# Optimization experiments

Measured on AMD Instinct MI355X. Metric: run time of the kernel, lower is better.

Reference implementation:

```python
import jax, jax.numpy as jnp
import numpy as np

N_NODES = 100000
N_EDGES = 1600000
D_FEAT = 64
D_HID = 128
N_HOP = 3


def setup_inputs() -> dict:
    key = jax.random.key(0)
    ks = jax.random.split(key, 7)
    nodes = jax.random.normal(ks[0], (N_NODES, D_FEAT), dtype=jnp.float32)
    senders = jax.random.randint(ks[1], (N_EDGES,), 0, N_NODES, dtype=jnp.int32)
    receivers = jax.random.randint(ks[2], (N_EDGES,), 0, N_NODES, dtype=jnp.int32)
    # per-hop MLP params (n_hop=3 independent layers), lecun-style scaling
    W1 = jax.random.normal(ks[3], (N_HOP, D_FEAT, D_HID), dtype=jnp.float32) / np.sqrt(D_FEAT)
    b1 = jnp.zeros((N_HOP, D_HID), dtype=jnp.float32)
    W2 = jax.random.normal(ks[4], (N_HOP, D_HID, D_FEAT), dtype=jnp.float32) / np.sqrt(D_HID)
    b2 = jnp.zeros((N_HOP, D_FEAT), dtype=jnp.float32)
    return {"nodes": nodes, "senders": senders, "receivers": receivers,
            "W1": W1, "b1": b1, "W2": W2, "b2": b2}


def _gcn_hop(x, senders, receivers, w1, b1, w2, b2):
    # update_node_fn: 2-layer MLP with leaky_relu between layers
    x = jax.nn.leaky_relu(jnp.dot(x, w1) + b1)
    x = jnp.dot(x, w2) + b2
    n = x.shape[0]
    ones = jnp.ones(senders.shape, dtype=x.dtype)
    send_deg = jax.ops.segment_sum(ones, senders, num_segments=n)
    recv_deg = jax.ops.segment_sum(ones, receivers, num_segments=n)
    # symmetric normalization: D_s^{-1/2} gather -> scatter-sum -> D_r^{-1/2}
    x = x * jax.lax.rsqrt(jnp.maximum(send_deg, 1.0))[:, None]
    x = jax.ops.segment_sum(x[senders], receivers, num_segments=n)
    x = x * jax.lax.rsqrt(jnp.maximum(recv_deg, 1.0))[:, None]
    return x


def reference(nodes, senders, receivers, W1, b1, W2, b2):
    x = nodes
    for i in range(N_HOP):
        x = _gcn_hop(x, senders, receivers, W1[i], b1[i], W2[i], b2[i])
    return x
```

## Files before the change

### kernel.cpp

```cpp
#include <hip/hip_runtime.h>

#define LRELU_SLOPE 0.01f
#define NBLK_A 512
#define BIN_SZ 256
#define MAXBIN 5120
#define NC2 128

typedef unsigned short ushort_t;
typedef unsigned int uint_t;

typedef float f32x4 __attribute__((ext_vector_type(4)));
typedef short bf16x8 __attribute__((ext_vector_type(8)));
#define MFMA16(a, b, c) __builtin_amdgcn_mfma_f32_16x16x32_bf16(a, b, c, 0, 0, 0)

__device__ inline uint_t f2bf(float f) {
    unsigned u = __float_as_uint(f);
    return (u + 0x7FFFu + ((u >> 16) & 1u)) >> 16;
}

__device__ inline void split2(float v, uint_t& hi, uint_t& lo) {
    hi = f2bf(v);
    float hif = __uint_as_float(hi << 16);
    lo = f2bf(v - hif);
}

__device__ inline float4 bf4_to_f4(ushort4 v) {
    float4 r;
    r.x = __uint_as_float((unsigned)v.x << 16);
    r.y = __uint_as_float((unsigned)v.y << 16);
    r.z = __uint_as_float((unsigned)v.z << 16);
    r.w = __uint_as_float((unsigned)v.w << 16);
    return r;
}

__device__ inline void acc_bf8(uint4 v, float* a) {
    a[0] += __uint_as_float(v.x << 16);
    a[1] += __uint_as_float(v.x & 0xFFFF0000u);
    a[2] += __uint_as_float(v.y << 16);
    a[3] += __uint_as_float(v.y & 0xFFFF0000u);
    a[4] += __uint_as_float(v.z << 16);
    a[5] += __uint_as_float(v.z & 0xFFFF0000u);
    a[6] += __uint_as_float(v.w << 16);
    a[7] += __uint_as_float(v.w & 0xFFFF0000u);
}

__device__ inline void acc_bf8m(uint4 v, float ok, float* a) {
    a[0] = fmaf(__uint_as_float(v.x << 16), ok, a[0]);
    a[1] = fmaf(__uint_as_float(v.x & 0xFFFF0000u), ok, a[1]);
    a[2] = fmaf(__uint_as_float(v.y << 16), ok, a[2]);
    a[3] = fmaf(__uint_as_float(v.y & 0xFFFF0000u), ok, a[3]);
    a[4] = fmaf(__uint_as_float(v.z << 16), ok, a[4]);
    a[5] = fmaf(__uint_as_float(v.z & 0xFFFF0000u), ok, a[5]);
    a[6] = fmaf(__uint_as_float(v.w << 16), ok, a[6]);
    a[7] = fmaf(__uint_as_float(v.w & 0xFFFF0000u), ok, a[7]);
}


__global__ __launch_bounds__(256) void build1_kernel(
        const float* __restrict__ W1, const float* __restrict__ W2,
        ushort_t* __restrict__ w1p, ushort_t* __restrict__ w2p,
        const int* __restrict__ receivers, int* __restrict__ cntA, int csA,
        const int* __restrict__ senders, uint_t* __restrict__ hist, int cs2,
        int e, int nbins, int half, int nwords) {
    __shared__ uint_t lds[12544];
    int bid = blockIdx.x, t = threadIdx.x;
    if (bid < 3) {
        int hop = bid;
        const float* w1 = W1 + hop * 64 * 128;
        const float* w2 = W2 + hop * 128 * 64;
        ushort_t* p1h = w1p + (size_t)hop * 16384;
        ushort_t* p1l = p1h + 8192;
        ushort_t* p2h = w2p + (size_t)hop * 16384;
        ushort_t* p2l = p2h + 8192;
        for (int i = t; i < 8192; i += 256) {
            int j = i & 7, o = (i >> 3) & 127, cq = i >> 10;
            int k = (cq >> 2) * 32 + (cq & 3) * 8 + j;
            uint_t h, l;
            split2(w1[k * 128 + o], h, l);
            p1h[i] = (ushort_t)h; p1l[i] = (ushort_t)l;
        }
        for (int i = t; i < 8192; i += 256) {
            int j = i & 7, o = (i >> 3) & 63, cq = i >> 9;
            int k = (cq >> 2) * 32 + (cq & 3) * 8 + j;
            uint_t h, l;
            split2(w2[k * 64 + o], h, l);
            p2h[i] = (ushort_t)h; p2l[i] = (ushort_t)l;
        }
    } else if (bid < 3 + NBLK_A) {
        int* cnt = (int*)lds;
        int b = bid - 3;
        for (int i = t; i < nbins; i += 256) cnt[i] = 0;
        __syncthreads();
        int base = b * csA, lim = min(csA, e - base);
        for (int i = t; i < lim; i += 256)
            atomicAdd(&cnt[receivers[base + i] >> 8], 1);
        __syncthreads();
        for (int i = t; i < nbins; i += 256) cntA[b * nbins + i] = cnt[i];
    } else {
        int idx = bid - 3 - NBLK_A;
        int c = idx >> 1;
        int h = idx & 1;
        int hw = half >> 2;
        for (int i = t; i < hw; i += 256) lds[i] = 0;
        __syncthreads();
        int base = c * cs2, lim = min(cs2, e - base);
        int lo = h * half;
        for (int i = t; i < lim; i += 256) {
            int v = senders[base + i] - lo;
            if ((unsigned)v < (unsigned)half)
                atomicAdd(&lds[v >> 2], 1u << ((v & 3) * 8));
        }
        __syncthreads();
        uint_t* d = hist + (size_t)c * nwords + (size_t)h * hw;
        for (int i = t; i < hw; i += 256) d[i] = lds[i];
    }
}


__global__ __launch_bounds__(512) void build2_kernel(
        const int* __restrict__ cntA, int* __restrict__ offT,
        int* __restrict__ binTot, int nbins,
        const uint_t* __restrict__ hist, int* __restrict__ deg,
        int nwords, int n) {
    __shared__ int s[NBLK_A];
    int bid = blockIdx.x, t = threadIdx.x;
    if (bid < nbins) {
        int bin = bid;
        int v = cntA[t * nbins + bin];
        s[t] = v;
        __syncthreads();
        for (int off = 1; off < NBLK_A; off <<= 1) {
            int add = (t >= off) ? s[t - off] : 0;
            __syncthreads();
            s[t] += add;
            __syncthreads();
        }
        offT[bin * NBLK_A + t] = s[t] - v;
        if (t == NBLK_A - 1) binTot[bin] = s[t];
    } else {
        int w = (bid - nbins) * 512 + t;
        if (w >= nwords) return;
        uint_t run = 0;
        for (int c = 0; c < NC2; c++) run += hist[(size_t)c * nwords + w];
        int v = w * 4;
        if (v + 3 < n) {
            ((int4*)deg)[w] = make_int4(run & 255, (run >> 8) & 255,
                                        (run >> 16) & 255, (int)(run >> 24));
        } else {
            for (int j = 0; j < 4 && v + j < n; j++) deg[v + j] = (run >> (8 * j)) & 255;
        }
    }
}

__global__ __launch_bounds__(512) void scanb_kernel(const int* __restrict__ binTot,
        int* __restrict__ binStart, int nbins) {
    __shared__ int s[512];
    int t = threadIdx.x;
    int v = (t < nbins) ? binTot[t] : 0;
    s[t] = v;
    __syncthreads();
    for (int off = 1; off < 512; off <<= 1) {
        int add = (t >= off) ? s[t - off] : 0;
        __syncthreads();
        s[t] += add;
        __syncthreads();
    }
    if (t < nbins) binStart[t] = s[t] - v;
    if (t == nbins - 1) binStart[nbins] = s[t];
}

__global__ __launch_bounds__(256) void binscat_kernel(const int* __restrict__ keys,
        const int* __restrict__ payload, const int* __restrict__ offT,
        const int* __restrict__ binStart,
        uint2* __restrict__ pairs, int cs, int e, int nbins) {
    __shared__ int cur[512];
    int b = blockIdx.x, t = threadIdx.x;
    for (int i = t; i < nbins; i += 256) cur[i] = offT[i * NBLK_A + b] + binStart[i];
    __syncthreads();
    int base = b * cs, lim = min(cs, e - base);
    for (int i = t; i < lim; i += 256) {
        int k = keys[base + i];
        int pl = payload[base + i];
        int pos = atomicAdd(&cur[k >> 8], 1);
        pairs[pos] = make_uint2((unsigned)k, (unsigned)pl);
    }
}

__global__ __launch_bounds__(256) void binsort_kernel(const uint2* __restrict__ pairs,
        const int* __restrict__ binStart, int* __restrict__ row_start,
        int* __restrict__ bucket, int nbins, int n, int e) {
    __shared__ int cnt[BIN_SZ];
    __shared__ int loc[BIN_SZ];
    __shared__ int buf[MAXBIN];
    int bin = blockIdx.x, t = threadIdx.x;
    int e0 = binStart[bin], e1 = binStart[bin + 1];
    int m = e1 - e0;
    if (m > MAXBIN) m = MAXBIN;
    cnt[t] = 0;
    __syncthreads();
    for (int i = t; i < m; i += 256)
        atomicAdd(&cnt[pairs[e0 + i].x & 255], 1);
    __syncthreads();
    int v = cnt[t];
    int node = bin * BIN_SZ + t;
    loc[t] = v;
    __syncthreads();
    for (int off = 1; off < BIN_SZ; off <<= 1) {
        int add = (t >= off) ? loc[t - off] : 0;
        __syncthreads();
        loc[t] += add;
        __syncthreads();
    }
    int excl = loc[t] - v;
    if (node < n) row_start[node] = e0 + excl;
    if (bin == nbins - 1 && t == 255) row_start[n] = e;
    cnt[t] = excl;
    __syncthreads();
    for (int i = t; i < m; i += 256) {
        uint2 pr = pairs[e0 + i];
        int pos = atomicAdd(&cnt[pr.x & 255], 1);
        buf[pos] = (int)pr.y;
    }
    __syncthreads();
    for (int i = t; i < m; i += 256) bucket[e0 + i] = buf[i];
}


template<int GATHER>
__global__ __launch_bounds__(512) void fused_mlp_kernel(const float* __restrict__ x,
        const ushort_t* __restrict__ yin, const int* __restrict__ rs,
        const int* __restrict__ bucket,
        const ushort_t* __restrict__ w1p, const float* __restrict__ b1g,
        const ushort_t* __restrict__ w2p, const float* __restrict__ b2g,
        const int* __restrict__ sdeg, ushort_t* __restrict__ y, int n) {
    __shared__ __align__(16) char smem[54272];
    ushort_t* xsh = (ushort_t*)smem;
    ushort_t* xsl = xsh + 4608;
    ushort_t* hsh = xsl + 4608;
    ushort_t* hsl = hsh + 8704;
    float* b1f   = (float*)(hsl + 8704);
    float* b2f   = b1f + 128;
    float* snorm = b2f + 64;
    float* ybuf  = (float*)smem;

    const ushort_t* w1ph = w1p;
    const ushort_t* w1pl = w1p + 8192;
    const ushort_t* w2ph = w2p;
    const ushort_t* w2pl = w2p + 8192;

    int tid = threadIdx.x;
    int nb = blockIdx.x * 64;

    if (tid < 32) ((float4*)b1f)[tid] = ((const float4*)b1g)[tid];
    else if (tid < 48) ((float4*)b2f)[tid - 32] = ((const float4*)b2g)[tid - 32];
    if (tid >= 448) {
        int t = tid - 448;
        int gn = nb + t;
        int d = (gn < n) ? sdeg[gn] : 1;
        snorm[t] = rsqrtf(fmaxf((float)d, 1.0f));
    }

    if (GATHER) {
        int node = tid >> 3, j = tid & 7;
        int gn = nb + node;
        float a[8];
        #pragma unroll
        for (int k = 0; k < 8; k++) a[k] = 0.f;
        if (gn < n) {
            int s0 = rs[gn];
            int deg = rs[gn + 1] - s0;
            const uint4* yrow = (const uint4*)yin;
            int i = 0;
            for (; i + 16 <= deg; i += 16) {
                int idx[16];
                #pragma unroll
                for (int k = 0; k < 16; k++) idx[k] = bucket[s0 + i + k];
                uint4 r0[16];
                #pragma unroll
                for (int k = 0; k < 16; k++) r0[k] = yrow[(size_t)idx[k] * 8 + j];
                #pragma unroll
                for (int k = 0; k < 16; k++) acc_bf8(r0[k], a);
            }
            for (; i < deg; i += 8) {
                int idx[8]; float ok[8];
                #pragma unroll
                for (int k = 0; k < 8; k++) {
                    int ii = i + k;
                    bool v = ii < deg;
                    idx[k] = bucket[v ? s0 + ii : s0];
                    ok[k] = v ? 1.0f : 0.0f;
                }
                uint4 rr[8];
                #pragma unroll
                for (int k = 0; k < 8; k++) rr[k] = yrow[(size_t)idx[k] * 8 + j];
                #pragma unroll
                for (int k = 0; k < 8; k++) acc_bf8m(rr[k], ok[k], a);
            }
            float sc = rsqrtf(fmaxf((float)deg, 1.0f));
            #pragma unroll
            for (int k = 0; k < 8; k++) a[k] *= sc;
        }
        uint_t h[8], l[8];
        #pragma unroll
        for (int k = 0; k < 8; k++) split2(a[k], h[k], l[k]);
        uint4 oh, ol;
        oh.x = h[0] | (h[1] << 16); oh.y = h[2] | (h[3] << 16);
        oh.z = h[4] | (h[5] << 16); oh.w = h[6] | (h[7] << 16);
        ol.x = l[0] | (l[1] << 16); ol.y = l[2] | (l[3] << 16);
        ol.z = l[4] | (l[5] << 16); ol.w = l[6] | (l[7] << 16);
        *(uint4*)&xsh[node * 72 + j * 8] = oh;
        *(uint4*)&xsl[node * 72 + j * 8] = ol;
    } else {
        for (int i = tid; i < 1024; i += 512) {
            int node = i >> 4, c4 = i & 15;
            int gn = nb + node;
            float4 v = make_float4(0.f, 0.f, 0.f, 0.f);
            if (gn < n) v = ((const float4*)x)[(size_t)gn * 16 + c4];
            uint_t h0, l0, h1, l1, h2, l2, h3, l3;
            split2(v.x, h0, l0); split2(v.y, h1, l1);
            split2(v.z, h2, l2); split2(v.w, h3, l3);
            *(uint2*)&xsh[node * 72 + c4 * 4] = make_uint2(h0 | (h1 << 16), h2 | (h3 << 16));
            *(uint2*)&xsl[node * 72 + c4 * 4] = make_uint2(l0 | (l1 << 16), l2 | (l3 << 16));
        }
    }
    __syncthreads();

    int w = tid >> 6, lane = tid & 63;
    int q = lane >> 4, m = lane & 15;
    int oq = w & 3, nh = w >> 2;
    bool even = ((m & 1) == 0);

    {
        f32x4 acc[2][2];
        #pragma unroll
        for (int a = 0; a < 2; a++)
            #pragma unroll
            for (int b = 0; b < 2; b++) acc[a][b] = (f32x4)(0.f);

        #pragma unroll
        for (int c = 0; c < 2; c++) {
            bf16x8 Ah[2], Al[2];
            #pragma unroll
            for (int nt = 0; nt < 2; nt++) {
                int node = nh * 32 + nt * 16 + m;
                Ah[nt] = *(const bf16x8*)&xsh[node * 72 + c * 32 + q * 8];
                Al[nt] = *(const bf16x8*)&xsl[node * 72 + c * 32 + q * 8];
            }
            #pragma unroll
            for (int ot = 0; ot < 2; ot++) {
                int o1 = oq * 32 + ot * 16 + m;
                size_t fo = (size_t)((c * 4 + q) * 128 + o1) * 8;
                bf16x8 Bh = *(const bf16x8*)&w1ph[fo];
                bf16x8 Bl = *(const bf16x8*)&w1pl[fo];
                #pragma unroll
                for (int nt = 0; nt < 2; nt++) {
                    acc[ot][nt] = MFMA16(Ah[nt], Bh, acc[ot][nt]);
                    acc[ot][nt] = MFMA16(Ah[nt], Bl, acc[ot][nt]);
                    acc[ot][nt] = MFMA16(Al[nt], Bh, acc[ot][nt]);
                }
            }
        }
        float b1v[2];
        b1v[0] = b1f[oq * 32 + m];
        b1v[1] = b1f[oq * 32 + 16 + m];
        #pragma unroll
        for (int ot = 0; ot < 2; ot++)
            #pragma unroll
            for (int nt = 0; nt < 2; nt++) {
                float hv[4], pv[4];
                #pragma unroll
                for (int r = 0; r < 4; r++) {
                    float t = acc[ot][nt][r] + b1v[ot];
                    hv[r] = (t > 0.f) ? t : LRELU_SLOPE * t;
                }
                #pragma unroll
                for (int r = 0; r < 4; r++) pv[r] = __shfl_xor(hv[r], 1, 64);
                int kpos = oq * 32 + ot * 16 + (m & ~1);
                #pragma unroll
                for (int rr = 0; rr < 2; rr++) {
                    int r = even ? rr : (2 + rr);
                    float vlo = even ? hv[r] : pv[r];
                    float vhi = even ? pv[r] : hv[r];
                    uint_t ah, al, bh, bl;
                    split2(vlo, ah, al);
                    split2(vhi, bh, bl);
                    int node = nh * 32 + nt * 16 + 4 * q + r;
                    *(uint_t*)&hsh[node * 136 + kpos] = ah | (bh << 16);
                    *(uint_t*)&hsl[node * 136 + kpos] = al | (bl << 16);
                }
            }
    }
    __syncthreads();

    {
        int ot2 = oq;
        f32x4 acc2[2];
        acc2[0] = (f32x4)(0.f);
        acc2[1] = (f32x4)(0.f);
        #pragma unroll
        for (int c = 0; c < 4; c++) {
            int o2 = ot2 * 16 + m;
            size_t fo = (size_t)((c * 4 + q) * 64 + o2) * 8;
            bf16x8 Bh = *(const bf16x8*)&w2ph[fo];
            bf16x8 Bl = *(const bf16x8*)&w2pl[fo];
            #pragma unroll
            for (int nt = 0; nt < 2; nt++) {
                int node = nh * 32 + nt * 16 + m;
                bf16x8 Ah = *(const bf16x8*)&hsh[node * 136 + c * 32 + q * 8];
                bf16x8 Al = *(const bf16x8*)&hsl[node * 136 + c * 32 + q * 8];
                acc2[nt] = MFMA16(Ah, Bh, acc2[nt]);
                acc2[nt] = MFMA16(Ah, Bl, acc2[nt]);
                acc2[nt] = MFMA16(Al, Bh, acc2[nt]);
            }
        }
        float b2v = b2f[ot2 * 16 + m];
        #pragma unroll
        for (int nt = 0; nt < 2; nt++)
            #pragma unroll
            for (int r = 0; r < 4; r++) {
                int node = nh * 32 + nt * 16 + 4 * q + r;
                float sn = snorm[node];
                ybuf[node * 68 + ot2 * 16 + m] = (acc2[nt][r] + b2v) * sn;
            }
    }
    __syncthreads();

    {
        int node = tid >> 3, c8 = tid & 7;
        int gn = nb + node;
        if (gn < n) {
            const float* src = &ybuf[node * 68 + c8 * 8];
            float4 v0 = *(const float4*)src;
            float4 v1 = *(const float4*)(src + 4);
            uint4 o;
            o.x = f2bf(v0.x) | (f2bf(v0.y) << 16);
            o.y = f2bf(v0.z) | (f2bf(v0.w) << 16);
            o.z = f2bf(v1.x) | (f2bf(v1.y) << 16);
            o.w = f2bf(v1.z) | (f2bf(v1.w) << 16);
            ((uint4*)y)[(size_t)gn * 8 + c8] = o;
        }
    }
}


__global__ __launch_bounds__(256) void agg_kernel(const ushort_t* __restrict__ y,
        const int* __restrict__ rs, const int* __restrict__ bucket,
        float* __restrict__ dst, int n) {
    int wid  = (blockIdx.x * 256 + threadIdx.x) >> 6;
    int lane = threadIdx.x & 63;
    int nd   = lane >> 5;
    int slot = (lane >> 4) & 1;
    int f4   = lane & 15;
    int node = wid * 2 + nd;
    if (node >= n) return;
    int s0  = rs[node];
    int deg = rs[node + 1] - s0;
    const ushort4* y4 = (const ushort4*)y;
    float4 acc = make_float4(0.f, 0.f, 0.f, 0.f);
    for (int i = slot; i < deg; i += 16) {
        int idx[8]; float ok[8];
        #pragma unroll
        for (int j = 0; j < 8; j++) {
            int ii = i + 2 * j;
            bool v = ii < deg;
            idx[j] = bucket[v ? s0 + ii : s0];
            ok[j] = v ? 1.0f : 0.0f;
        }
        #pragma unroll
        for (int j = 0; j < 8; j++) {
            float4 v4 = bf4_to_f4(y4[(size_t)idx[j] * 16 + f4]);
            acc.x = fmaf(v4.x, ok[j], acc.x);
            acc.y = fmaf(v4.y, ok[j], acc.y);
            acc.z = fmaf(v4.z, ok[j], acc.z);
            acc.w = fmaf(v4.w, ok[j], acc.w);
        }
    }
    acc.x += __shfl_xor(acc.x, 16, 64);
    acc.y += __shfl_xor(acc.y, 16, 64);
    acc.z += __shfl_xor(acc.z, 16, 64);
    acc.w += __shfl_xor(acc.w, 16, 64);
    if (slot == 0) {
        float sc = rsqrtf(fmaxf((float)deg, 1.0f));
        acc.x *= sc; acc.y *= sc; acc.z *= sc; acc.w *= sc;
        ((float4*)dst)[(size_t)node * 16 + f4] = acc;
    }
}


extern "C" void kernel_launch(void* const* d_in, const int* in_sizes, int n_in,
                              void* d_out, int out_size, void* d_ws, size_t ws_size,
                              hipStream_t stream) {
    const float* nodes     = (const float*)d_in[0];
    const int*   senders   = (const int*)d_in[1];
    const int*   receivers = (const int*)d_in[2];
    const float* W1 = (const float*)d_in[3];
    const float* b1 = (const float*)d_in[4];
    const float* W2 = (const float*)d_in[5];
    const float* b2 = (const float*)d_in[6];

    int N = in_sizes[0] / 64;
    int E = in_sizes[1];
    int NBINS = (N + BIN_SZ - 1) / BIN_SZ;
    int CSA = (E + NBLK_A - 1) / NBLK_A;
    int CS2 = (E + NC2 - 1) / NC2;
    int HALF = ((N + 7) / 8) * 4;
    int NW2 = 2 * (HALF >> 2);

    char* p = (char*)d_ws;
    auto carve = [&](size_t bytes) -> char* {
        char* r = p;
        p += (bytes + 255) & ~(size_t)255;
        return r;
    };
    ushort_t* yA   = (ushort_t*)carve((size_t)N * 64 * 2);
    ushort_t* yB   = (ushort_t*)carve((size_t)N * 64 * 2);
    int*      rs   = (int*)carve((size_t)(N + 1) * 4);
    int*      sdeg = (int*)carve((size_t)N * 4);
    int*      bucket = (int*)carve((size_t)E * 4);
    int*      binStart = (int*)carve((size_t)(NBINS + 1) * 4);
    int*      binTot   = (int*)carve((size_t)NBINS * 4);
    ushort_t* w1p  = (ushort_t*)carve((size_t)3 * 16384 * 2);
    ushort_t* w2p  = (ushort_t*)carve((size_t)3 * 16384 * 2);
    char* scratch  = carve((size_t)E * 8 + 2 * (size_t)NBLK_A * NBINS * 4 + 4096);
    uint2* pairs = (uint2*)scratch;
    int*   cntA  = (int*)(scratch + (size_t)E * 8);
    int*   offT  = cntA + (size_t)NBLK_A * NBINS;
    uint_t* T1   = (uint_t*)pairs;

    build1_kernel<<<3 + NBLK_A + NC2 * 2, 256, 0, stream>>>(
            W1, W2, w1p, w2p, receivers, cntA, CSA,
            senders, T1, CS2, E, NBINS, HALF, NW2);
    build2_kernel<<<NBINS + (NW2 + 511) / 512, 512, 0, stream>>>(
            cntA, offT, binTot, NBINS, T1, sdeg, NW2, N);
    scanb_kernel<<<1, 512, 0, stream>>>(binTot, binStart, NBINS);
    binscat_kernel<<<NBLK_A, 256, 0, stream>>>(receivers, senders, offT, binStart, pairs, CSA, E, NBINS);
    binsort_kernel<<<NBINS, 256, 0, stream>>>(pairs, binStart, rs, bucket, NBINS, N, E);

    int mbf = (N + 63) / 64;
    int agg_blocks = (N / 2 + 4) / 4 + 1;

    fused_mlp_kernel<0><<<mbf, 512, 0, stream>>>(nodes, nullptr, nullptr, nullptr,
            w1p, b1, w2p, b2, sdeg, yA, N);
    fused_mlp_kernel<1><<<mbf, 512, 0, stream>>>(nullptr, yA, rs, bucket,
            w1p + 16384, b1 + 128, w2p + 16384, b2 + 64, sdeg, yB, N);
    fused_mlp_kernel<1><<<mbf, 512, 0, stream>>>(nullptr, yB, rs, bucket,
            w1p + 32768, b1 + 256, w2p + 32768, b2 + 128, sdeg, yA, N);
    agg_kernel<<<agg_blocks, 256, 0, stream>>>(yA, rs, bucket, (float*)d_out, N);
}
```

Baseline: 330.9 us.

## Build CSR via per-node degree histograms and global atomic scatter

Replaces the two-level bin-partition sort (bin counts, per-bin offsets, pair scatter, per-bin local sort) with receiver degree histograms computed the same way as sender degrees. A scan then gives row starts, and edges are scattered into buckets through global atomicAdd on per-node cursors. This removes the intermediate pairs buffer and the binsort pass, but it adds heavy global atomic contention and produces a nondeterministic order of edges within each row. That ordering could change floating-point summation order in later aggregation.

```diff
diff --git a/kernel.cpp b/kernel.cpp
--- a/kernel.cpp
+++ b/kernel.cpp
@@ -1,9 +1,6 @@
 #include <hip/hip_runtime.h>
 
 #define LRELU_SLOPE 0.01f
-#define NBLK_A 512
-#define BIN_SZ 256
-#define MAXBIN 5120
 #define NC2 128
 
 typedef unsigned short ushort_t;
@@ -59,9 +56,9 @@
 __global__ __launch_bounds__(256) void build1_kernel(
         const float* __restrict__ W1, const float* __restrict__ W2,
         ushort_t* __restrict__ w1p, ushort_t* __restrict__ w2p,
-        const int* __restrict__ receivers, int* __restrict__ cntA, int csA,
-        const int* __restrict__ senders, uint_t* __restrict__ hist, int cs2,
-        int e, int nbins, int half, int nwords) {
+        const int* __restrict__ receivers, uint_t* __restrict__ histR,
+        const int* __restrict__ senders, uint_t* __restrict__ histS,
+        int cs2, int e, int half, int nwords) {
     __shared__ uint_t lds[12544];
     int bid = blockIdx.x, t = threadIdx.x;
     if (bid < 3) {
@@ -86,78 +83,83 @@
             split2(w2[k * 64 + o], h, l);
             p2h[i] = (ushort_t)h; p2l[i] = (ushort_t)l;
         }
-    } else if (bid < 3 + NBLK_A) {
-        int* cnt = (int*)lds;
-        int b = bid - 3;
-        for (int i = t; i < nbins; i += 256) cnt[i] = 0;
-        __syncthreads();
-        int base = b * csA, lim = min(csA, e - base);
-        for (int i = t; i < lim; i += 256)
-            atomicAdd(&cnt[receivers[base + i] >> 8], 1);
-        __syncthreads();
-        for (int i = t; i < nbins; i += 256) cntA[b * nbins + i] = cnt[i];
-    } else {
-        int idx = bid - 3 - NBLK_A;
-        int c = idx >> 1;
-        int h = idx & 1;
-        int hw = half >> 2;
-        for (int i = t; i < hw; i += 256) lds[i] = 0;
-        __syncthreads();
-        int base = c * cs2, lim = min(cs2, e - base);
-        int lo = h * half;
-        for (int i = t; i < lim; i += 256) {
-            int v = senders[base + i] - lo;
-            if ((unsigned)v < (unsigned)half)
-                atomicAdd(&lds[v >> 2], 1u << ((v & 3) * 8));
-        }
-        __syncthreads();
-        uint_t* d = hist + (size_t)c * nwords + (size_t)h * hw;
-        for (int i = t; i < hw; i += 256) d[i] = lds[i];
-    }
+        return;
+    }
+    int role = bid - 3;
+    const int* keys = (role < NC2 * 2) ? receivers : senders;
+    uint_t* hist    = (role < NC2 * 2) ? histR : histS;
+    int idx = (role < NC2 * 2) ? role : role - NC2 * 2;
+    int c = idx >> 1;
+    int h = idx & 1;
+    int hw = half >> 2;
+    for (int i = t; i < hw; i += 256) lds[i] = 0;
+    __syncthreads();
+    int base = c * cs2, lim = min(cs2, e - base);
+    int lo = h * half;
+    for (int i = t; i < lim; i += 256) {
+        int v = keys[base + i] - lo;
+        if ((unsigned)v < (unsigned)half)
+            atomicAdd(&lds[v >> 2], 1u << ((v & 3) * 8));
+    }
+    __syncthreads();
+    uint_t* d = hist + (size_t)c * nwords + (size_t)h * hw;
+    for (int i = t; i < hw; i += 256) d[i] = lds[i];
 }
 
 
 __global__ __launch_bounds__(512) void build2_kernel(
-        const int* __restrict__ cntA, int* __restrict__ offT,
-        int* __restrict__ binTot, int nbins,
-        const uint_t* __restrict__ hist, int* __restrict__ deg,
-        int nwords, int n) {
-    __shared__ int s[NBLK_A];
+        const uint_t* __restrict__ histS, int* __restrict__ sdeg,
+        const uint_t* __restrict__ histR, int* __restrict__ rdeg,
+        int* __restrict__ partials, int ks, int nwords, int n) {
+    __shared__ int s[512];
     int bid = blockIdx.x, t = threadIdx.x;
-    if (bid < nbins) {
-        int bin = bid;
-        int v = cntA[t * nbins + bin];
-        s[t] = v;
-        __syncthreads();
-        for (int off = 1; off < NBLK_A; off <<= 1) {
-            int add = (t >= off) ? s[t - off] : 0;
-            __syncthreads();
-            s[t] += add;
-            __syncthreads();
-        }
-        offT[bin * NBLK_A + t] = s[t] - v;
-        if (t == NBLK_A - 1) binTot[bin] = s[t];
-    } else {
-        int w = (bid - nbins) * 512 + t;
+    if (bid < ks) {
+        int w = bid * 512 + t;
         if (w >= nwords) return;
         uint_t run = 0;
-        for (int c = 0; c < NC2; c++) run += hist[(size_t)c * nwords + w];
+        for (int c = 0; c < NC2; c++) run += histS[(size_t)c * nwords + w];
         int v = w * 4;
         if (v + 3 < n) {
-            ((int4*)deg)[w] = make_int4(run & 255, (run >> 8) & 255,
-                                        (run >> 16) & 255, (int)(run >> 24));
+            ((int4*)sdeg)[w] = make_int4(run & 255, (run >> 8) & 255,
+                                         (run >> 16) & 255, (int)(run >> 24));
         } else {
-            for (int j = 0; j < 4 && v + j < n; j++) deg[v + j] = (run >> (8 * j)) & 255;
-        }
-    }
-}
-
-__global__ __launch_bounds__(512) void scanb_kernel(const int* __restrict__ binTot,
-        int* __restrict__ binStart, int nbins) {
+            for (int j = 0; j < 4 && v + j < n; j++) sdeg[v + j] = (run >> (8 * j)) & 255;
+        }
+    } else {
+        int b2 = bid - ks;
+        int w = b2 * 512 + t;
+        uint_t run = 0;
+        if (w < nwords)
+            for (int c = 0; c < NC2; c++) run += histR[(size_t)c * nwords + w];
+        int d0 = run & 255, d1 = (run >> 8) & 255, d2 = (run >> 16) & 255, d3 = (int)(run >> 24);
+        if (w < nwords) ((int4*)rdeg)[w] = make_int4(d0, d1, d2, d3);
+        s[t] = d0 + d1 + d2 + d3;
+        __syncthreads();
+        for (int off = 256; off > 0; off >>= 1) {
+            if (t < off) s[t] += s[t + off];
+            __syncthreads();
+        }
+        if (t == 0) partials[b2] = s[0];
+    }
+}
+
+
+__global__ __launch_bounds__(512) void scan2_kernel(const int* __restrict__ rdeg,
+        const int* __restrict__ partials, int* __restrict__ rs, int* __restrict__ cursor,
+        int ks, int nwords, int n, int e) {
     __shared__ int s[512];
-    int t = threadIdx.x;
-    int v = (t < nbins) ? binTot[t] : 0;
-    s[t] = v;
+    __shared__ int ps[64];
+    int b = blockIdx.x, t = threadIdx.x;
+    if (t < 64) ps[t] = (t < ks) ? partials[t] : 0;
+    __syncthreads();
+    int base = 0;
+    for (int i = 0; i < b; i++) base += ps[i];
+    __syncthreads();
+    int w = b * 512 + t;
+    int4 d = make_int4(0, 0, 0, 0);
+    if (w < nwords) d = ((const int4*)rdeg)[w];
+    int tot = d.x + d.y + d.z + d.w;
+    s[t] = tot;
     __syncthreads();
     for (int off = 1; off < 512; off <<= 1) {
         int add = (t >= off) ? s[t - off] : 0;
@@ -165,64 +167,33 @@
         s[t] += add;
         __syncthreads();
     }
-    if (t < nbins) binStart[t] = s[t] - v;
-    if (t == nbins - 1) binStart[nbins] = s[t];
-}
-
-__global__ __launch_bounds__(256) void binscat_kernel(const int* __restrict__ keys,
-        const int* __restrict__ payload, const int* __restrict__ offT,
-        const int* __restrict__ binStart,
-        uint2* __restrict__ pairs, int cs, int e, int nbins) {
-    __shared__ int cur[512];
+    int excl = base + s[t] - tot;
+    if (w < nwords) {
+        int v = w * 4;
+        int r0 = excl, r1 = r0 + d.x, r2 = r1 + d.y, r3 = r2 + d.z;
+        if (v + 3 < n) {
+            ((int4*)rs)[w] = make_int4(r0, r1, r2, r3);
+            ((int4*)cursor)[w] = make_int4(r0, r1, r2, r3);
+        } else {
+            int rr[4] = {r0, r1, r2, r3};
+            for (int j = 0; j < 4 && v + j < n; j++) { rs[v + j] = rr[j]; cursor[v + j] = rr[j]; }
+        }
+    }
+    if (b == 0 && t == 0) rs[n] = e;
+}
+
+
+__global__ __launch_bounds__(256) void scatter_kernel(const int* __restrict__ receivers,
+        const int* __restrict__ senders, int* __restrict__ cursor,
+        int* __restrict__ bucket, int cs, int e) {
     int b = blockIdx.x, t = threadIdx.x;
-    for (int i = t; i < nbins; i += 256) cur[i] = offT[i * NBLK_A + b] + binStart[i];
-    __syncthreads();
     int base = b * cs, lim = min(cs, e - base);
     for (int i = t; i < lim; i += 256) {
-        int k = keys[base + i];
-        int pl = payload[base + i];
-        int pos = atomicAdd(&cur[k >> 8], 1);
-        pairs[pos] = make_uint2((unsigned)k, (unsigned)pl);
-    }
-}
-
-__global__ __launch_bounds__(256) void binsort_kernel(const uint2* __restrict__ pairs,
-        const int* __restrict__ binStart, int* __restrict__ row_start,
-        int* __restrict__ bucket, int nbins, int n, int e) {
-    __shared__ int cnt[BIN_SZ];
-    __shared__ int loc[BIN_SZ];
-    __shared__ int buf[MAXBIN];
-    int bin = blockIdx.x, t = threadIdx.x;
-    int e0 = binStart[bin], e1 = binStart[bin + 1];
-    int m = e1 - e0;
-    if (m > MAXBIN) m = MAXBIN;
-    cnt[t] = 0;
-    __syncthreads();
-    for (int i = t; i < m; i += 256)
-        atomicAdd(&cnt[pairs[e0 + i].x & 255], 1);
-    __syncthreads();
-    int v = cnt[t];
-    int node = bin * BIN_SZ + t;
-    loc[t] = v;
-    __syncthreads();
-    for (int off = 1; off < BIN_SZ; off <<= 1) {
-        int add = (t >= off) ? loc[t - off] : 0;
-        __syncthreads();
-        loc[t] += add;
-        __syncthreads();
-    }
-    int excl = loc[t] - v;
-    if (node < n) row_start[node] = e0 + excl;
-    if (bin == nbins - 1 && t == 255) row_start[n] = e;
-    cnt[t] = excl;
-    __syncthreads();
-    for (int i = t; i < m; i += 256) {
-        uint2 pr = pairs[e0 + i];
-        int pos = atomicAdd(&cnt[pr.x & 255], 1);
-        buf[pos] = (int)pr.y;
-    }
-    __syncthreads();
-    for (int i = t; i < m; i += 256) bucket[e0 + i] = buf[i];
+        int r = receivers[base + i];
+        int sv = senders[base + i];
+        int pos = atomicAdd(&cursor[r], 1);
+        bucket[pos] = sv;
+    }
 }
 
 
@@ -500,11 +471,11 @@
 
     int N = in_sizes[0] / 64;
     int E = in_sizes[1];
-    int NBINS = (N + BIN_SZ - 1) / BIN_SZ;
-    int CSA = (E + NBLK_A - 1) / NBLK_A;
     int CS2 = (E + NC2 - 1) / NC2;
     int HALF = ((N + 7) / 8) * 4;
     int NW2 = 2 * (HALF >> 2);
+    int KS = (NW2 + 511) / 512;
+    int CSE = (E + 511) / 512;
 
     char* p = (char*)d_ws;
     auto carve = [&](size_t bytes) -> char* {
@@ -514,27 +485,24 @@
     };
     ushort_t* yA   = (ushort_t*)carve((size_t)N * 64 * 2);
     ushort_t* yB   = (ushort_t*)carve((size_t)N * 64 * 2);
-    int*      rs   = (int*)carve((size_t)(N + 1) * 4);
-    int*      sdeg = (int*)carve((size_t)N * 4);
+    int*      rs   = (int*)carve((size_t)(N + 4) * 4);
+    int*      cursor = (int*)carve((size_t)(N + 4) * 4);
+    int*      sdeg = (int*)carve((size_t)N * 4 + 16);
+    int*      rdeg = (int*)carve((size_t)NW2 * 16);
     int*      bucket = (int*)carve((size_t)E * 4);
-    int*      binStart = (int*)carve((size_t)(NBINS + 1) * 4);
-    int*      binTot   = (int*)carve((size_t)NBINS * 4);
+    int*      partials = (int*)carve(256 * 4);
     ushort_t* w1p  = (ushort_t*)carve((size_t)3 * 16384 * 2);
     ushort_t* w2p  = (ushort_t*)carve((size_t)3 * 16384 * 2);
-    char* scratch  = carve((size_t)E * 8 + 2 * (size_t)NBLK_A * NBINS * 4 + 4096);
-    uint2* pairs = (uint2*)scratch;
-    int*   cntA  = (int*)(scratch + (size_t)E * 8);
-    int*   offT  = cntA + (size_t)NBLK_A * NBINS;
-    uint_t* T1   = (uint_t*)pairs;
-
-    build1_kernel<<<3 + NBLK_A + NC2 * 2, 256, 0, stream>>>(
-            W1, W2, w1p, w2p, receivers, cntA, CSA,
-            senders, T1, CS2, E, NBINS, HALF, NW2);
-    build2_kernel<<<NBINS + (NW2 + 511) / 512, 512, 0, stream>>>(
-            cntA, offT, binTot, NBINS, T1, sdeg, NW2, N);
-    scanb_kernel<<<1, 512, 0, stream>>>(binTot, binStart, NBINS);
-    binscat_kernel<<<NBLK_A, 256, 0, stream>>>(receivers, senders, offT, binStart, pairs, CSA, E, NBINS);
-    binsort_kernel<<<NBINS, 256, 0, stream>>>(pairs, binStart, rs, bucket, NBINS, N, E);
+    uint_t* histR = (uint_t*)carve((size_t)NC2 * NW2 * 4);
+    uint_t* histS = (uint_t*)carve((size_t)NC2 * NW2 * 4);
+
+    build1_kernel<<<3 + NC2 * 2 + NC2 * 2, 256, 0, stream>>>(
+            W1, W2, w1p, w2p, receivers, histR, senders, histS,
+            CS2, E, HALF, NW2);
+    build2_kernel<<<2 * KS, 512, 0, stream>>>(
+            histS, sdeg, histR, rdeg, partials, KS, NW2, N);
+    scan2_kernel<<<KS, 512, 0, stream>>>(rdeg, partials, rs, cursor, KS, NW2, N, E);
+    scatter_kernel<<<512, 256, 0, stream>>>(receivers, senders, cursor, bucket, CSE, E);
 
     int mbf = (N + 63) / 64;
     int agg_blocks = (N / 2 + 4) / 4 + 1;
```

Result: slower. 426.3 us (+28.8%).
